# Optimization experiments

Measured on AMD Instinct MI355X. Metric: run time of the kernel, lower is better.

Reference implementation:

```python
import jax, jax.numpy as jnp
import numpy as np
import math

N_NODES = 100000
N_EDGES = 1600000
IN_FEATS = 128
H_FEATS = 64
NUM_CLASSES = 2
D = 2  # num_layers -> d+1 = 3 filters, each polynomial of degree d


def _calc_thetas(d):
    # Beta-Bernstein polynomial coefficients, ascending powers of x.
    # f_i(x) = (x/2)^i (1-x/2)^(d-i) / B(i+1, d+1-i),  B = i!(d-i)!/(d+1)!
    thetas = []
    for i in range(d + 1):
        beta = math.factorial(i) * math.factorial(d - i) / math.factorial(d + 1)
        p = np.array([1.0])
        for _ in range(i):
            p = np.convolve(p, [0.0, 0.5])
        for _ in range(d - i):
            p = np.convolve(p, [1.0, -0.5])
        thetas.append([float(c) for c in (p / beta)])
    return thetas

THETAS = _calc_thetas(D)


def setup_inputs() -> dict:
    key = jax.random.key(0)
    ks = jax.random.split(key, 12)
    x = jax.random.normal(ks[0], (N_NODES, IN_FEATS), dtype=jnp.float32)
    edge_index = jax.random.randint(ks[1], (2, N_EDGES), 0, N_NODES, dtype=jnp.int64)
    s = 0.05
    W1 = jax.random.normal(ks[2], (IN_FEATS, H_FEATS), jnp.float32) * s
    b1 = jnp.zeros((H_FEATS,), jnp.float32)
    W2 = jax.random.normal(ks[3], (H_FEATS, H_FEATS), jnp.float32) * s
    b2 = jnp.zeros((H_FEATS,), jnp.float32)
    Wm1 = jax.random.normal(ks[4], (H_FEATS * len(THETAS), H_FEATS), jnp.float32) * s
    bm1 = jnp.zeros((H_FEATS,), jnp.float32)
    Wm2 = jax.random.normal(ks[5], (H_FEATS, NUM_CLASSES), jnp.float32) * s
    bm2 = jnp.zeros((NUM_CLASSES,), jnp.float32)
    return {"x": x, "edge_index": edge_index, "W1": W1, "b1": b1,
            "W2": W2, "b2": b2, "Wm1": Wm1, "bm1": bm1, "Wm2": Wm2, "bm2": bm2}


def reference(x, edge_index, W1, b1, W2, b2, Wm1, bm1, Wm2, bm2):
    N = x.shape[0]
    src, dst = edge_index[0], edge_index[1]
    # in-degrees (edges point src -> dst, message summed at dst)
    deg = jax.ops.segment_sum(jnp.ones((edge_index.shape[1],), x.dtype), dst,
                              num_segments=N)
    dinv = jnp.clip(deg, 1.0, None) ** -0.5  # [N]
    dinv = dinv[:, None]
    # two linear + ReLU layers
    h = jax.nn.relu(x @ W1 + b1)
    h = jax.nn.relu(h @ W2 + b2)
    # PolyConv per theta: feat <- feat - D^-1/2 A D^-1/2 feat; acc += theta_k feat
    outs = []
    for theta in THETAS:
        feat = h
        acc = theta[0] * feat
        for k in range(1, len(theta)):
            msg = jax.ops.segment_sum((feat * dinv)[src], dst, num_segments=N)
            feat = feat - msg * dinv
            acc = acc + theta[k] * feat
        outs.append(acc)
    h_final = jnp.concatenate(outs, axis=-1)  # [N, h_feats*(d+1)]
    # MLP (2 layers): Linear -> ReLU -> Linear
    h_final = jax.nn.relu(h_final @ Wm1 + bm1)
    return h_final @ Wm2 + bm2
```

## Files before the change

### kernel.cpp

```cpp
#include <hip/hip_runtime.h>
#include <math.h>

#define N_NODES 100000
#define N_EDGES 1600000
#define IN_F 128
#define H_F 64

#define NBKT 391
#define BSEG 5120
#define BCAP 5120

#define NP        100096
#define OFF_CNT   0
#define OFF_MPK   512
#define OFF_W1H   6656
#define OFF_W1L   10752
#define OFF_W2H   14848
#define OFF_W2L   16896
#define OFF_OFFS  18944
#define OFF_D2    (OFF_OFFS + NP + 64)
#define OFF_RD    (OFF_D2 + NP)
#define OFF_DINV  (OFF_RD + NP)
#define OFF_ADJ   (OFF_DINV + NP)
#define OFF_H0    (OFF_ADJ + N_EDGES)
#define OFF_H1    (OFF_H0 + N_NODES*32)
#define OFF_H2    (OFF_H1 + N_NODES*32)

typedef __attribute__((ext_vector_type(8))) short bf16x8;
typedef __attribute__((ext_vector_type(4))) float f32x4;
typedef __attribute__((ext_vector_type(2))) float f32x2;

__device__ __forceinline__ unsigned short bf16rn(float f) {
    unsigned u = __float_as_uint(f);
    u += 0x7FFFu + ((u >> 16) & 1u);
    return (unsigned short)(u >> 16);
}
#define UNPK(u, lo, hi) { lo = __uint_as_float((u) << 16); hi = __uint_as_float((u) & 0xFFFF0000u); }
#define ACC2(u, A) { f32x2 t_; t_.x = __uint_as_float((u) << 16); \
                     t_.y = __uint_as_float((u) & 0xFFFF0000u); A += t_; }

__global__ __launch_bounds__(256) void k_prep(const float* __restrict__ Wm1,
        const float* __restrict__ W1, const float* __restrict__ W2,
        unsigned short* __restrict__ mpk,
        unsigned short* __restrict__ w1h, unsigned short* __restrict__ w1l,
        unsigned short* __restrict__ w2h, unsigned short* __restrict__ w2l,
        int* __restrict__ cnt) {
    int idx = blockIdx.x * 256 + threadIdx.x;
    if (idx < 512) cnt[idx] = 0;
    if (idx < 12288) {
        int j = idx & 7;
        int n = (idx >> 3) & 63;
        int qd = (idx >> 9) & 3;
        int s = idx >> 11;
        int k = s * 32 + qd * 8 + j;
        int p = k >> 6;
        int kk = k & 63;
        float w0 = Wm1[kk * 64 + n];
        float w1 = Wm1[(64 + kk) * 64 + n];
        float w2 = Wm1[(128 + kk) * 64 + n];
        float v;
        if (p == 0)      v = 3.0f * w0;
        else if (p == 1) v = 3.0f * (w1 - w0);
        else             v = 0.75f * (w0 + w2) - 1.5f * w1;
        mpk[idx] = bf16rn(v);
    } else if (idx < 12288 + 8192) {
        int lin = idx - 12288;
        int j = lin & 7, cc = (lin >> 3) & 15, ot = (lin >> 7) & 3;
        int qd = (lin >> 9) & 3, ks = lin >> 11;
        float v = W1[(ks * 32 + qd * 8 + j) * 64 + ot * 16 + cc];
        unsigned short h = bf16rn(v);
        w1h[lin] = h;
        w1l[lin] = bf16rn(v - __uint_as_float((unsigned)h << 16));
    } else if (idx < 24576) {
        int lin = idx - 20480;
        int j = lin & 7, cc = (lin >> 3) & 15, ot = (lin >> 7) & 3;
        int qd = (lin >> 9) & 3, ks = lin >> 11;
        float v = W2[(ks * 32 + qd * 8 + j) * 64 + ot * 16 + cc];
        unsigned short h = bf16rn(v);
        w2h[lin] = h;
        w2l[lin] = bf16rn(v - __uint_as_float((unsigned)h << 16));
    }
}

__global__ __launch_bounds__(256) void k_bin(const int* __restrict__ src,
        const int* __restrict__ dst, int* __restrict__ cnt,
        int* __restrict__ binned, int E) {
    __shared__ int hist[4][NBKT + 1];
    __shared__ int cur4[4][NBKT + 1];
    int t = threadIdx.x;
    int w = t >> 6;
    for (int i = t; i < 4 * (NBKT + 1); i += 256) (&hist[0][0])[i] = 0;
    __syncthreads();
    int base = blockIdx.x * 8192 + t;
    int d[32];
    #pragma unroll
    for (int i = 0; i < 32; ++i) {
        int e = base + i * 256;
        int dd = (e < E) ? dst[e] : -1;
        d[i] = dd;
        if (dd >= 0) atomicAdd(&hist[w][dd >> 8], 1);
    }
    __syncthreads();
    for (int i = t; i < NBKT; i += 256) {
        int h0 = hist[0][i], h1 = hist[1][i], h2 = hist[2][i], h3 = hist[3][i];
        int tot = h0 + h1 + h2 + h3;
        int b0 = (tot > 0) ? atomicAdd(&cnt[i], tot) : 0;
        cur4[0][i] = b0;
        cur4[1][i] = b0 + h0;
        cur4[2][i] = b0 + h0 + h1;
        cur4[3][i] = b0 + h0 + h1 + h2;
    }
    __syncthreads();
    #pragma unroll
    for (int i = 0; i < 32; ++i) {
        int e = base + i * 256;
        if (e < E) {
            int s = src[e];
            int dd = d[i];
            int b = dd >> 8;
            int p = atomicAdd(&cur4[w][b], 1);
            if (p < BSEG) binned[b * BSEG + p] = ((dd & 255) << 17) | s;
        }
    }
}

__global__ __launch_bounds__(256) void k_cfill(const int* __restrict__ binned,
        const int* __restrict__ cnt, int* __restrict__ offs, int* __restrict__ adj,
        float* __restrict__ d2a, float* __restrict__ rda, float* __restrict__ dinva) {
    __shared__ int csum[256];
    __shared__ int degl[256];
    __shared__ int curl[256];
    __shared__ int wsum[4];
    __shared__ int adjl[BCAP];
    int b = blockIdx.x, t = threadIdx.x;
    int p = 0;
    if (2 * t < NBKT) p += cnt[2 * t];
    if (2 * t + 1 < NBKT) p += cnt[2 * t + 1];
    csum[t] = p;
    __syncthreads();
    #pragma unroll
    for (int off = 1; off < 256; off <<= 1) {
        int u = (t >= off) ? csum[t - off] : 0;
        __syncthreads();
        csum[t] += u;
        __syncthreads();
    }
    int b2 = b >> 1;
    int baseb = ((b2 > 0) ? csum[b2 - 1] : 0) + ((b & 1) ? cnt[b - 1] : 0);
    int cntb = cnt[b];
    if (b == 0 && t == 0) offs[N_NODES] = N_EDGES;
    int n0 = b << 8;
    const int* bp = binned + b * BSEG;
    degl[t] = 0;
    __syncthreads();
    for (int i = t; i < cntb; i += 256) atomicAdd(&degl[bp[i] >> 17], 1);
    __syncthreads();
    int d0 = degl[t];
    int lane = t & 63, wid = t >> 6;
    int inc = d0;
    #pragma unroll
    for (int off = 1; off < 64; off <<= 1) {
        int v = __shfl_up(inc, off, 64);
        if (lane >= off) inc += v;
    }
    if (lane == 63) wsum[wid] = inc;
    __syncthreads();
    int wb = 0;
    for (int w = 0; w < wid; ++w) wb += wsum[w];
    int excl = wb + inc - d0;
    curl[t] = excl;
    int n = n0 + t;
    if (n < N_NODES) {
        offs[n] = baseb + excl;
        float df = (float)d0;
        if (df < 1.f) df = 1.f;
        float di = 1.0f / sqrtf(df);
        dinva[n] = di;
        d2a[n] = di * di;
        rda[n] = sqrtf(df);
    }
    __syncthreads();
    for (int i = t; i < cntb; i += 256) {
        int w = bp[i];
        int loc = w >> 17;
        int s = w & 0x1FFFF;
        int pp = atomicAdd(&curl[loc], 1);
        if (pp < BCAP) adjl[pp] = s;
        else adj[baseb + pp] = s << 7;
    }
    __syncthreads();
    int lim = cntb < BCAP ? cntb : BCAP;
    for (int i = t; i < lim; i += 256) adj[baseb + i] = adjl[i] << 7;
}

__global__ __launch_bounds__(256) void k_gemm12(const float* __restrict__ x,
        const unsigned short* __restrict__ w1h, const unsigned short* __restrict__ w1l,
        const unsigned short* __restrict__ w2h, const unsigned short* __restrict__ w2l,
        const float* __restrict__ b1, const float* __restrict__ b2,
        const float* __restrict__ dinva, unsigned short* __restrict__ gsh, int N) {
    __shared__ unsigned int Hl[4][16 * 65];
    __shared__ unsigned short Sl[4][16 * 66];
    int t = threadIdx.x;
    int w = t >> 6, lane = t & 63;
    int c = lane & 15, qd = lane >> 4;
    int nbase = blockIdx.x * 64 + w * 16;
    if (nbase >= N) return;
    int node = nbase + c;
    int nclamp = (node < N) ? node : N - 1;

    f32x4 a0 = {0.f,0.f,0.f,0.f}, a1 = a0, a2 = a0, a3 = a0;
    #pragma unroll
    for (int ks = 0; ks < 4; ++ks) {
        const float* xp = x + (size_t)nclamp * IN_F + ks * 32 + qd * 8;
        float4 xa = *(const float4*)xp;
        float4 xb = *(const float4*)(xp + 4);
        float xs[8] = {xa.x, xa.y, xa.z, xa.w, xb.x, xb.y, xb.z, xb.w};
        bf16x8 ahi, alo;
        #pragma unroll
        for (int j = 0; j < 8; ++j) {
            unsigned short h = bf16rn(xs[j]);
            ahi[j] = (short)h;
            alo[j] = (short)bf16rn(xs[j] - __uint_as_float((unsigned)h << 16));
        }
        const unsigned short* bh = w1h + (size_t)(ks * 4 + qd) * 512;
        const unsigned short* bl = w1l + (size_t)(ks * 4 + qd) * 512;
        bf16x8 h0 = *(const bf16x8*)(bh + 0 * 128 + c * 8);
        bf16x8 l0 = *(const bf16x8*)(bl + 0 * 128 + c * 8);
        bf16x8 h1 = *(const bf16x8*)(bh + 1 * 128 + c * 8);
        bf16x8 l1 = *(const bf16x8*)(bl + 1 * 128 + c * 8);
        bf16x8 h2 = *(const bf16x8*)(bh + 2 * 128 + c * 8);
        bf16x8 l2 = *(const bf16x8*)(bl + 2 * 128 + c * 8);
        bf16x8 h3 = *(const bf16x8*)(bh + 3 * 128 + c * 8);
        bf16x8 l3 = *(const bf16x8*)(bl + 3 * 128 + c * 8);
        a0 = __builtin_amdgcn_mfma_f32_16x16x32_bf16(ahi, h0, a0, 0, 0, 0);
        a1 = __builtin_amdgcn_mfma_f32_16x16x32_bf16(ahi, h1, a1, 0, 0, 0);
        a2 = __builtin_amdgcn_mfma_f32_16x16x32_bf16(ahi, h2, a2, 0, 0, 0);
        a3 = __builtin_amdgcn_mfma_f32_16x16x32_bf16(ahi, h3, a3, 0, 0, 0);
        a0 = __builtin_amdgcn_mfma_f32_16x16x32_bf16(alo, h0, a0, 0, 0, 0);
        a1 = __builtin_amdgcn_mfma_f32_16x16x32_bf16(alo, h1, a1, 0, 0, 0);
        a2 = __builtin_amdgcn_mfma_f32_16x16x32_bf16(alo, h2, a2, 0, 0, 0);
        a3 = __builtin_amdgcn_mfma_f32_16x16x32_bf16(alo, h3, a3, 0, 0, 0);
        a0 = __builtin_amdgcn_mfma_f32_16x16x32_bf16(ahi, l0, a0, 0, 0, 0);
        a1 = __builtin_amdgcn_mfma_f32_16x16x32_bf16(ahi, l1, a1, 0, 0, 0);
        a2 = __builtin_amdgcn_mfma_f32_16x16x32_bf16(ahi, l2, a2, 0, 0, 0);
        a3 = __builtin_amdgcn_mfma_f32_16x16x32_bf16(ahi, l3, a3, 0, 0, 0);
    }
    #pragma unroll
    for (int ot = 0; ot < 4; ++ot) {
        float bb = b1[ot * 16 + c];
        f32x4 a = (ot == 0) ? a0 : (ot == 1) ? a1 : (ot == 2) ? a2 : a3;
        #pragma unroll
        for (int r = 0; r < 4; ++r) {
            float h = fmaxf(a[r] + bb, 0.f);
            unsigned short hh = bf16rn(h);
            unsigned short hl = bf16rn(h - __uint_as_float((unsigned)hh << 16));
            Hl[w][(qd * 4 + r) * 65 + ot * 16 + c] = ((unsigned)hh << 16) | hl;
        }
    }
    f32x4 d0 = {0.f,0.f,0.f,0.f}, d1 = d0, d2 = d0, d3 = d0;
    #pragma unroll
    for (int ks = 0; ks < 2; ++ks) {
        bf16x8 ahi, alo;
        #pragma unroll
        for (int j = 0; j < 8; ++j) {
            unsigned v = Hl[w][c * 65 + ks * 32 + qd * 8 + j];
            ahi[j] = (short)(v >> 16);
            alo[j] = (short)(v & 0xFFFFu);
        }
        const unsigned short* bh = w2h + (size_t)(ks * 4 + qd) * 512;
        const unsigned short* bl = w2l + (size_t)(ks * 4 + qd) * 512;
        bf16x8 h0 = *(const bf16x8*)(bh + 0 * 128 + c * 8);
        bf16x8 l0 = *(const bf16x8*)(bl + 0 * 128 + c * 8);
        bf16x8 h1 = *(const bf16x8*)(bh + 1 * 128 + c * 8);
        bf16x8 l1 = *(const bf16x8*)(bl + 1 * 128 + c * 8);
        bf16x8 h2 = *(const bf16x8*)(bh + 2 * 128 + c * 8);
        bf16x8 l2 = *(const bf16x8*)(bl + 2 * 128 + c * 8);
        bf16x8 h3 = *(const bf16x8*)(bh + 3 * 128 + c * 8);
        bf16x8 l3 = *(const bf16x8*)(bl + 3 * 128 + c * 8);
        d0 = __builtin_amdgcn_mfma_f32_16x16x32_bf16(ahi, h0, d0, 0, 0, 0);
        d1 = __builtin_amdgcn_mfma_f32_16x16x32_bf16(ahi, h1, d1, 0, 0, 0);
        d2 = __builtin_amdgcn_mfma_f32_16x16x32_bf16(ahi, h2, d2, 0, 0, 0);
        d3 = __builtin_amdgcn_mfma_f32_16x16x32_bf16(ahi, h3, d3, 0, 0, 0);
        d0 = __builtin_amdgcn_mfma_f32_16x16x32_bf16(alo, h0, d0, 0, 0, 0);
        d1 = __builtin_amdgcn_mfma_f32_16x16x32_bf16(alo, h1, d1, 0, 0, 0);
        d2 = __builtin_amdgcn_mfma_f32_16x16x32_bf16(alo, h2, d2, 0, 0, 0);
        d3 = __builtin_amdgcn_mfma_f32_16x16x32_bf16(alo, h3, d3, 0, 0, 0);
        d0 = __builtin_amdgcn_mfma_f32_16x16x32_bf16(ahi, l0, d0, 0, 0, 0);
        d1 = __builtin_amdgcn_mfma_f32_16x16x32_bf16(ahi, l1, d1, 0, 0, 0);
        d2 = __builtin_amdgcn_mfma_f32_16x16x32_bf16(ahi, l2, d2, 0, 0, 0);
        d3 = __builtin_amdgcn_mfma_f32_16x16x32_bf16(ahi, l3, d3, 0, 0, 0);
    }
    #pragma unroll
    for (int ot = 0; ot < 4; ++ot) {
        float bb = b2[ot * 16 + c];
        f32x4 a = (ot == 0) ? d0 : (ot == 1) ? d1 : (ot == 2) ? d2 : d3;
        #pragma unroll
        for (int r = 0; r < 4; ++r) {
            int nd = nbase + qd * 4 + r;
            float di = dinva[(nd < N) ? nd : N - 1];
            Sl[w][(qd * 4 + r) * 66 + ot * 16 + c] = bf16rn(di * fmaxf(a[r] + bb, 0.f));
        }
    }
    #pragma unroll
    for (int i = 0; i < 4; ++i) {
        int nl = i * 4 + qd;
        int nd = nbase + nl;
        if (nd < N) {
            ushort4 v;
            v.x = Sl[w][nl * 66 + c * 4 + 0];
            v.y = Sl[w][nl * 66 + c * 4 + 1];
            v.z = Sl[w][nl * 66 + c * 4 + 2];
            v.w = Sl[w][nl * 66 + c * 4 + 3];
            *(ushort4*)(gsh + (size_t)nd * 64 + c * 4) = v;
        }
    }
}

__global__ __launch_bounds__(256) void k_prop(const unsigned short* __restrict__ gh,
        unsigned short* __restrict__ gout, const int* __restrict__ offs,
        const int* __restrict__ adjb, const float* __restrict__ d2a, int N) {
    int t = threadIdx.x;
    int lane = t & 63;
    int q = lane & 7;
    int g = (lane >> 3) & 1;
    int n = blockIdx.x * 16 + (t >> 6) * 4 + (lane >> 4);
    int nc = (n < N) ? n : N - 1;
    int beg = offs[nc], end = offs[nc + 1];
    float d2n = d2a[nc];
    const char* base = (const char*)gh;
    uint4 sv = *(const uint4*)(gh + (size_t)nc * 64 + 8 * q);
    f32x2 A0 = {0.f, 0.f}, A1 = A0, A2 = A0, A3 = A0;
    unsigned qo = (unsigned)(q << 4);
    int e = beg + g;
    bool pa0 = e < end;
    bool pa1 = e + 2 < end;
    unsigned off0 = 0, off1 = 0;
    if (pa0) off0 = (unsigned)adjb[e];
    if (pa1) off1 = (unsigned)adjb[e + 2];
    uint4 v0, v1;
    if (pa0) v0 = *(const uint4*)(base + (size_t)(off0 + qo));
    if (pa1) v1 = *(const uint4*)(base + (size_t)(off1 + qo));
    int en = e + 4;
    bool pv = pa1;
    while (pv) {
        bool pa2 = en < end;
        unsigned off2 = 0;
        if (pa2) off2 = (unsigned)adjb[en];
        ACC2(v0.x, A0); ACC2(v0.y, A1); ACC2(v0.z, A2); ACC2(v0.w, A3);
        v0 = v1;
        pv = pa2;
        if (pv) v1 = *(const uint4*)(base + (size_t)(off2 + qo));
        en += 2;
    }
    if (pa0) { ACC2(v0.x, A0); ACC2(v0.y, A1); ACC2(v0.z, A2); ACC2(v0.w, A3); }
    A0.x += __shfl_xor(A0.x, 8); A0.y += __shfl_xor(A0.y, 8);
    A1.x += __shfl_xor(A1.x, 8); A1.y += __shfl_xor(A1.y, 8);
    A2.x += __shfl_xor(A2.x, 8); A2.y += __shfl_xor(A2.y, 8);
    A3.x += __shfl_xor(A3.x, 8); A3.y += __shfl_xor(A3.y, 8);
    if (g == 0 && n < N) {
        float l, h;
        uint4 r;
        UNPK(sv.x, l, h);
        r.x = ((unsigned)bf16rn(fmaf(-d2n, A0.y, h)) << 16) | bf16rn(fmaf(-d2n, A0.x, l));
        UNPK(sv.y, l, h);
        r.y = ((unsigned)bf16rn(fmaf(-d2n, A1.y, h)) << 16) | bf16rn(fmaf(-d2n, A1.x, l));
        UNPK(sv.z, l, h);
        r.z = ((unsigned)bf16rn(fmaf(-d2n, A2.y, h)) << 16) | bf16rn(fmaf(-d2n, A2.x, l));
        UNPK(sv.w, l, h);
        r.w = ((unsigned)bf16rn(fmaf(-d2n, A3.y, h)) << 16) | bf16rn(fmaf(-d2n, A3.x, l));
        *(uint4*)(gout + (size_t)n * 64 + 8 * q) = r;
    }
}

__global__ __launch_bounds__(256) void k_final(const unsigned short* __restrict__ g0h,
        const unsigned short* __restrict__ g1h, const unsigned short* __restrict__ g2h,
        const unsigned short* __restrict__ mpk, const float* __restrict__ bm1,
        const float* __restrict__ Wm2, const float* __restrict__ bm2,
        const float* __restrict__ rda, float* __restrict__ out, int N) {
    int t = threadIdx.x;
    int w = t >> 6, lane = t & 63;
    int c = lane & 15, qd = lane >> 4;
    int nbase = blockIdx.x * 64 + w * 16;
    if (nbase >= N) return;
    int node = nbase + c;
    int nclamp = (node < N) ? node : N - 1;
    const unsigned short* bufs[3] = {g0h, g1h, g2h};
    f32x4 acc0 = {0.f, 0.f, 0.f, 0.f};
    f32x4 acc1 = {0.f, 0.f, 0.f, 0.f};
    f32x4 acc2 = {0.f, 0.f, 0.f, 0.f};
    f32x4 acc3 = {0.f, 0.f, 0.f, 0.f};
    #pragma unroll
    for (int s = 0; s < 6; ++s) {
        const unsigned short* gp = bufs[s >> 1];
        int k0 = (s & 1) * 32;
        bf16x8 a = *(const bf16x8*)(gp + (size_t)nclamp * 64 + k0 + qd * 8);
        const unsigned short* mb = mpk + (size_t)((s * 4 + qd) * 64) * 8;
        bf16x8 b0 = *(const bf16x8*)(mb + (size_t)(c) * 8);
        bf16x8 b1 = *(const bf16x8*)(mb + (size_t)(16 + c) * 8);
        bf16x8 b2 = *(const bf16x8*)(mb + (size_t)(32 + c) * 8);
        bf16x8 b3 = *(const bf16x8*)(mb + (size_t)(48 + c) * 8);
        acc0 = __builtin_amdgcn_mfma_f32_16x16x32_bf16(a, b0, acc0, 0, 0, 0);
        acc1 = __builtin_amdgcn_mfma_f32_16x16x32_bf16(a, b1, acc1, 0, 0, 0);
        acc2 = __builtin_amdgcn_mfma_f32_16x16x32_bf16(a, b2, acc2, 0, 0, 0);
        acc3 = __builtin_amdgcn_mfma_f32_16x16x32_bf16(a, b3, acc3, 0, 0, 0);
    }
    float rdr[4];
    #pragma unroll
    for (int r = 0; r < 4; ++r) {
        int nd = nbase + qd * 4 + r;
        rdr[r] = rda[(nd < N) ? nd : N - 1];
    }
    float p0[4] = {0.f, 0.f, 0.f, 0.f};
    float p1[4] = {0.f, 0.f, 0.f, 0.f};
    #pragma unroll
    for (int ot = 0; ot < 4; ++ot) {
        int col = ot * 16 + c;
        float bmc = bm1[col];
        float wc0 = Wm2[col * 2 + 0];
        float wc1 = Wm2[col * 2 + 1];
        f32x4 a = (ot == 0) ? acc0 : (ot == 1) ? acc1 : (ot == 2) ? acc2 : acc3;
        #pragma unroll
        for (int r = 0; r < 4; ++r) {
            float h = fmaxf(fmaf(rdr[r], a[r], bmc), 0.f);
            p0[r] = fmaf(h, wc0, p0[r]);
            p1[r] = fmaf(h, wc1, p1[r]);
        }
    }
    #pragma unroll
    for (int m = 1; m < 16; m <<= 1) {
        #pragma unroll
        for (int r = 0; r < 4; ++r) {
            p0[r] += __shfl_xor(p0[r], m);
            p1[r] += __shfl_xor(p1[r], m);
        }
    }
    if (c == 0) {
        float bo0 = bm2[0], bo1 = bm2[1];
        #pragma unroll
        for (int r = 0; r < 4; ++r) {
            int nd = nbase + qd * 4 + r;
            if (nd < N) {
                float2 o;
                o.x = p0[r] + bo0;
                o.y = p1[r] + bo1;
                *(float2*)(out + (size_t)nd * 2) = o;
            }
        }
    }
}

extern "C" void kernel_launch(void* const* d_in, const int* in_sizes, int n_in,
                              void* d_out, int out_size, void* d_ws, size_t ws_size,
                              hipStream_t stream) {
    const float* x   = (const float*)d_in[0];
    const int*   ei  = (const int*)d_in[1];
    const float* W1  = (const float*)d_in[2];
    const float* b1  = (const float*)d_in[3];
    const float* W2  = (const float*)d_in[4];
    const float* b2  = (const float*)d_in[5];
    const float* Wm1 = (const float*)d_in[6];
    const float* bm1 = (const float*)d_in[7];
    const float* Wm2 = (const float*)d_in[8];
    const float* bm2 = (const float*)d_in[9];
    float* out = (float*)d_out;

    int* ws = (int*)d_ws;
    int*   cnt   = ws + OFF_CNT;
    unsigned short* mpk = (unsigned short*)(ws + OFF_MPK);
    unsigned short* w1h = (unsigned short*)(ws + OFF_W1H);
    unsigned short* w1l = (unsigned short*)(ws + OFF_W1L);
    unsigned short* w2h = (unsigned short*)(ws + OFF_W2H);
    unsigned short* w2l = (unsigned short*)(ws + OFF_W2L);
    int*   offs  = ws + OFF_OFFS;
    float* d2a   = (float*)(ws + OFF_D2);
    float* rda   = (float*)(ws + OFF_RD);
    float* dinva = (float*)(ws + OFF_DINV);
    int*   adj   = ws + OFF_ADJ;
    unsigned short* gs0h = (unsigned short*)(ws + OFF_H0);
    unsigned short* gs1h = (unsigned short*)(ws + OFF_H1);
    unsigned short* gs2h = (unsigned short*)(ws + OFF_H2);
    int*   binned = ws + OFF_H1;

    const int* srcp = ei;
    const int* dstp = ei + N_EDGES;

    k_prep<<<96, 256, 0, stream>>>(Wm1, W1, W2, mpk, w1h, w1l, w2h, w2l, cnt);
    k_bin<<<(N_EDGES + 8191) / 8192, 256, 0, stream>>>(srcp, dstp, cnt, binned, N_EDGES);
    k_cfill<<<NBKT, 256, 0, stream>>>(binned, cnt, offs, adj, d2a, rda, dinva);

    int nblk = (N_NODES + 63) / 64;
    k_gemm12<<<nblk, 256, 0, stream>>>(x, w1h, w1l, w2h, w2l, b1, b2, dinva, gs0h, N_NODES);

    k_prop<<<(N_NODES + 15) / 16, 256, 0, stream>>>(gs0h, gs1h, offs, adj, d2a, N_NODES);
    k_prop<<<(N_NODES + 15) / 16, 256, 0, stream>>>(gs1h, gs2h, offs, adj, d2a, N_NODES);

    k_final<<<nblk, 256, 0, stream>>>(gs0h, gs1h, gs2h, mpk, bm1, Wm2, bm2, rda, out, N_NODES);
}
```

Baseline: 235.8 us.

## Fuse second propagation step into final MLP kernel via shared memory

The second sparse propagation and the final MLP kernel are merged into one kernel. Each block computes the propagated features for 16 nodes into shared memory, then one wave runs the MFMA MLP on them. This removes one launch and the global write and re-read of the third feature buffer. In exchange, the MLP stage uses only 64 of 256 threads per block, and each block now covers 16 nodes instead of 64, so mpk weights are re-read by four times as many blocks.

```diff
diff --git a/kernel.cpp b/kernel.cpp
--- a/kernel.cpp
+++ b/kernel.cpp
@@ -372,28 +372,86 @@
     }
 }
 
-__global__ __launch_bounds__(256) void k_final(const unsigned short* __restrict__ g0h,
-        const unsigned short* __restrict__ g1h, const unsigned short* __restrict__ g2h,
+__global__ __launch_bounds__(256) void k_propf(const unsigned short* __restrict__ gh,
+        const unsigned short* __restrict__ g0h, const int* __restrict__ offs,
+        const int* __restrict__ adjb, const float* __restrict__ d2a,
         const unsigned short* __restrict__ mpk, const float* __restrict__ bm1,
         const float* __restrict__ Wm2, const float* __restrict__ bm2,
         const float* __restrict__ rda, float* __restrict__ out, int N) {
+    __shared__ unsigned short g2l[16][72];
     int t = threadIdx.x;
-    int w = t >> 6, lane = t & 63;
+    int lane = t & 63;
+    int q = lane & 7;
+    int g = (lane >> 3) & 1;
+    int ln = (t >> 6) * 4 + (lane >> 4);
+    int nbase = blockIdx.x * 16;
+    int n = nbase + ln;
+    int nc = (n < N) ? n : N - 1;
+    int beg = offs[nc], end = offs[nc + 1];
+    float d2n = d2a[nc];
+    const char* base = (const char*)gh;
+    uint4 sv = *(const uint4*)(gh + (size_t)nc * 64 + 8 * q);
+    f32x2 A0 = {0.f, 0.f}, A1 = A0, A2 = A0, A3 = A0;
+    unsigned qo = (unsigned)(q << 4);
+    int e = beg + g;
+    bool pa0 = e < end;
+    bool pa1 = e + 2 < end;
+    unsigned off0 = 0, off1 = 0;
+    if (pa0) off0 = (unsigned)adjb[e];
+    if (pa1) off1 = (unsigned)adjb[e + 2];
+    uint4 v0, v1;
+    if (pa0) v0 = *(const uint4*)(base + (size_t)(off0 + qo));
+    if (pa1) v1 = *(const uint4*)(base + (size_t)(off1 + qo));
+    int en = e + 4;
+    bool pv = pa1;
+    while (pv) {
+        bool pa2 = en < end;
+        unsigned off2 = 0;
+        if (pa2) off2 = (unsigned)adjb[en];
+        ACC2(v0.x, A0); ACC2(v0.y, A1); ACC2(v0.z, A2); ACC2(v0.w, A3);
+        v0 = v1;
+        pv = pa2;
+        if (pv) v1 = *(const uint4*)(base + (size_t)(off2 + qo));
+        en += 2;
+    }
+    if (pa0) { ACC2(v0.x, A0); ACC2(v0.y, A1); ACC2(v0.z, A2); ACC2(v0.w, A3); }
+    A0.x += __shfl_xor(A0.x, 8); A0.y += __shfl_xor(A0.y, 8);
+    A1.x += __shfl_xor(A1.x, 8); A1.y += __shfl_xor(A1.y, 8);
+    A2.x += __shfl_xor(A2.x, 8); A2.y += __shfl_xor(A2.y, 8);
+    A3.x += __shfl_xor(A3.x, 8); A3.y += __shfl_xor(A3.y, 8);
+    if (g == 0) {
+        float l, h;
+        uint4 r;
+        UNPK(sv.x, l, h);
+        r.x = ((unsigned)bf16rn(fmaf(-d2n, A0.y, h)) << 16) | bf16rn(fmaf(-d2n, A0.x, l));
+        UNPK(sv.y, l, h);
+        r.y = ((unsigned)bf16rn(fmaf(-d2n, A1.y, h)) << 16) | bf16rn(fmaf(-d2n, A1.x, l));
+        UNPK(sv.z, l, h);
+        r.z = ((unsigned)bf16rn(fmaf(-d2n, A2.y, h)) << 16) | bf16rn(fmaf(-d2n, A2.x, l));
+        UNPK(sv.w, l, h);
+        r.w = ((unsigned)bf16rn(fmaf(-d2n, A3.y, h)) << 16) | bf16rn(fmaf(-d2n, A3.x, l));
+        *(uint4*)(&g2l[ln][q * 8]) = r;
+    }
+    __syncthreads();
+    if (t >= 64) return;
+
     int c = lane & 15, qd = lane >> 4;
-    int nbase = blockIdx.x * 64 + w * 16;
-    if (nbase >= N) return;
     int node = nbase + c;
     int nclamp = (node < N) ? node : N - 1;
-    const unsigned short* bufs[3] = {g0h, g1h, g2h};
+    int lc = nclamp - nbase;
     f32x4 acc0 = {0.f, 0.f, 0.f, 0.f};
     f32x4 acc1 = {0.f, 0.f, 0.f, 0.f};
     f32x4 acc2 = {0.f, 0.f, 0.f, 0.f};
     f32x4 acc3 = {0.f, 0.f, 0.f, 0.f};
     #pragma unroll
     for (int s = 0; s < 6; ++s) {
-        const unsigned short* gp = bufs[s >> 1];
-        int k0 = (s & 1) * 32;
-        bf16x8 a = *(const bf16x8*)(gp + (size_t)nclamp * 64 + k0 + qd * 8);
+        bf16x8 a;
+        if (s < 4) {
+            const unsigned short* gp = (s < 2) ? g0h : gh;
+            a = *(const bf16x8*)(gp + (size_t)nclamp * 64 + (s & 1) * 32 + qd * 8);
+        } else {
+            a = *(const bf16x8*)(&g2l[lc][(s & 1) * 32 + qd * 8]);
+        }
         const unsigned short* mb = mpk + (size_t)((s * 4 + qd) * 64) * 8;
         bf16x8 b0 = *(const bf16x8*)(mb + (size_t)(c) * 8);
         bf16x8 b1 = *(const bf16x8*)(mb + (size_t)(16 + c) * 8);
@@ -478,7 +536,6 @@
     int*   adj   = ws + OFF_ADJ;
     unsigned short* gs0h = (unsigned short*)(ws + OFF_H0);
     unsigned short* gs1h = (unsigned short*)(ws + OFF_H1);
-    unsigned short* gs2h = (unsigned short*)(ws + OFF_H2);
     int*   binned = ws + OFF_H1;
 
     const int* srcp = ei;
@@ -492,7 +549,6 @@
     k_gemm12<<<nblk, 256, 0, stream>>>(x, w1h, w1l, w2h, w2l, b1, b2, dinva, gs0h, N_NODES);
 
     k_prop<<<(N_NODES + 15) / 16, 256, 0, stream>>>(gs0h, gs1h, offs, adj, d2a, N_NODES);
-    k_prop<<<(N_NODES + 15) / 16, 256, 0, stream>>>(gs1h, gs2h, offs, adj, d2a, N_NODES);
-
-    k_final<<<nblk, 256, 0, stream>>>(gs0h, gs1h, gs2h, mpk, bm1, Wm2, bm2, rda, out, N_NODES);
-}
+    k_propf<<<(N_NODES + 15) / 16, 256, 0, stream>>>(gs1h, gs0h, offs, adj, d2a,
+            mpk, bm1, Wm2, bm2, rda, out, N_NODES);
+}
```

Result: no change. 237.1 us (+0.5%).
